# Kernel optimization log

Measured on AMD Instinct MI355X. Metric: run time of the kernel, lower is better.

The kernel has to match this reference:

```python
import jax, jax.numpy as jnp
import numpy as np

B, T, E, H, D = 4, 2048, 1024, 16, 64  # batch, seq(block_size), n_embed, num_heads, hidden_dim


def setup_inputs() -> dict:
    key = jax.random.key(0)
    ks = jax.random.split(key, 10)
    s_in = 1.0 / np.sqrt(E)
    return {
        "x": jax.random.normal(ks[0], (B, T, E), dtype=jnp.float32),
        "Wq": jax.random.normal(ks[1], (H, E, D), dtype=jnp.float32) * s_in,
        "bq": jnp.zeros((H, D), dtype=jnp.float32),
        "Wk": jax.random.normal(ks[2], (H, E, D), dtype=jnp.float32) * s_in,
        "bk": jnp.zeros((H, D), dtype=jnp.float32),
        "Wv": jax.random.normal(ks[3], (H, E, D), dtype=jnp.float32) * s_in,
        "bv": jnp.zeros((H, D), dtype=jnp.float32),
        "Wp": jax.random.normal(ks[4], (E, E), dtype=jnp.float32) * s_in,
        "bp": jnp.zeros((E,), dtype=jnp.float32),
    }


def reference(x, Wq, bq, Wk, bk, Wv, bv, Wp, bp):
    # Batched equivalent of the per-head Python loop: each head h computes
    # causal scaled-dot-product attention with its own Q/K/V projections.
    q = jnp.einsum("bte,hed->bhtd", x, Wq) + bq[None, :, None, :]
    k = jnp.einsum("bte,hed->bhtd", x, Wk) + bk[None, :, None, :]
    v = jnp.einsum("bte,hed->bhtd", x, Wv) + bv[None, :, None, :]
    scale = 1.0 / jnp.sqrt(jnp.asarray(D, dtype=x.dtype))
    scores = jnp.einsum("bhtd,bhsd->bhts", q, k) * scale  # [B,H,T,T]
    causal = jnp.tril(jnp.ones((T, T), dtype=bool))
    scores = jnp.where(causal[None, None, :, :], scores, jnp.asarray(-jnp.inf, dtype=x.dtype))
    att = jax.nn.softmax(scores, axis=-1)
    head_out = jnp.einsum("bhts,bhsd->bhtd", att, v)  # [B,H,T,D]
    # concat heads along last dim: [B,T,H*D] == [B,T,E]
    cat = head_out.transpose(0, 2, 1, 3).reshape(B, T, H * D)
    out = cat @ Wp + bp  # final projection (dropout is identity in eval)
    return out
```

## Files before the change

kernel.cpp:

```cpp
#include <hip/hip_runtime.h>


typedef __attribute__((ext_vector_type(8))) __bf16 bf16x8;
typedef __attribute__((ext_vector_type(4))) float f32x4;
typedef __attribute__((ext_vector_type(16))) float f32x16;
typedef __attribute__((ext_vector_type(4))) unsigned int u32x4;
typedef __attribute__((ext_vector_type(2))) unsigned int u32x2;
typedef unsigned short u16;
typedef unsigned int u32;

#define DEV __device__ __forceinline__

#define QK_SCALE 0.18033688011112042f

DEV u16 f2bf(float f) {
  u32 u = __builtin_bit_cast(u32, f);
  u += 0x7fffu + ((u >> 16) & 1u);
  return (u16)(u >> 16);
}
DEV u32 pack2(float a, float b) { return (u32)f2bf(a) | ((u32)f2bf(b) << 16); }

DEV float exp2_hw(float x) { float r; asm("v_exp_f32 %0, %1" : "=v"(r) : "v"(x)); return r; }
DEV u32 cvtpk_bf16(float lo, float hi) {
  u32 r; asm("v_cvt_pk_bf16_f32 %0, %1, %2" : "=v"(r) : "v"(lo), "v"(hi)); return r;
}
DEV void pl32swap(u32& a, u32& b) { asm("v_permlane32_swap_b32 %0, %1" : "+v"(a), "+v"(b)); }
DEV float max3f(float a, float b, float c) {
  float r; asm("v_max3_f32 %0, %1, %2, %3" : "=v"(r) : "v"(a), "v"(b), "v"(c)); return r;
}

DEV f32x16 zero16() { f32x16 z;
#pragma unroll
  for (int i = 0; i < 16; i++) z[i] = 0.f;
  return z; }

DEV void gll16(const u16* g, u16* l) {
  __builtin_amdgcn_global_load_lds((const __attribute__((address_space(1))) void*)g,
                                   (__attribute__((address_space(3))) void*)l, 16, 0, 0);
}

#define SCHEDB() __builtin_amdgcn_sched_barrier(0)
#define FENCE4()  do { asm volatile("s_waitcnt vmcnt(4) lgkmcnt(0)" ::: "memory"); SCHEDB(); \
                       __builtin_amdgcn_s_barrier(); SCHEDB(); } while (0)
#define FENCE0()  do { asm volatile("s_waitcnt vmcnt(0) lgkmcnt(0)" ::: "memory"); SCHEDB(); \
                       __builtin_amdgcn_s_barrier(); SCHEDB(); } while (0)

__global__ __launch_bounds__(256) void prep_all_kernel(
    const float* __restrict__ x, const float* __restrict__ bq, const float* __restrict__ bk,
    const float* __restrict__ bv, const float* __restrict__ Wq, const float* __restrict__ Wk,
    const float* __restrict__ Wv, const float* __restrict__ Wp,
    u16* __restrict__ xbf, float* __restrict__ bqkv, u16* __restrict__ wqkvT, u16* __restrict__ wpT) {
  __shared__ float t[64][65];
  int bidAll = blockIdx.x, tid = threadIdx.x;
  if (bidAll < 4096) {
    int gid = bidAll * 256 + tid;
    if (gid < 3072) {
      float v = (gid < 1024) ? bq[gid] * QK_SCALE : (gid < 2048 ? bk[gid - 1024] : bv[gid - 2048]);
      bqkv[gid] = v;
    }
    const float4* xv = (const float4*)x;
    float4 f0 = xv[(size_t)gid * 2];
    float4 f1 = xv[(size_t)gid * 2 + 1];
    u32x4 st;
    st.x = pack2(f0.x, f0.y); st.y = pack2(f0.z, f0.w);
    st.z = pack2(f1.x, f1.y); st.w = pack2(f1.z, f1.w);
    *(u32x4*)&xbf[(size_t)gid * 8] = st;
    return;
  }
  int bid = bidAll - 4096;
  int r0 = tid >> 6, c = tid & 63;
  if (bid < 768) {
    int p = bid >> 8, rem = bid & 255, h = rem >> 4, et = rem & 15;
    float sc = (p == 0) ? QK_SCALE : 1.0f;
    const float* src = (p == 0 ? Wq : (p == 1 ? Wk : Wv)) + ((size_t)h * 1024 + et * 64) * 64;
#pragma unroll
    for (int i = 0; i < 16; i++) { int e = r0 + i * 4; t[e][c] = src[(size_t)e * 64 + c]; }
    __syncthreads();
    u16* dst = wqkvT + ((size_t)p * 1024 + h * 64) * 1024 + et * 64;
#pragma unroll
    for (int i = 0; i < 16; i++) { int d = r0 + i * 4; dst[(size_t)d * 1024 + c] = f2bf(t[c][d] * sc); }
  } else {
    int b2 = bid - 768, rt = b2 >> 4, ct = b2 & 15;
#pragma unroll
    for (int i = 0; i < 16; i++) { int e = r0 + i * 4; t[e][c] = Wp[(size_t)(rt * 64 + e) * 1024 + ct * 64 + c]; }
    __syncthreads();
#pragma unroll
    for (int i = 0; i < 16; i++) { int f = r0 + i * 4; wpT[(size_t)(ct * 64 + f) * 1024 + rt * 64 + c] = f2bf(t[c][f]); }
  }
}

DEV void stage_tile32(const u16* __restrict__ X, int row0, int k0, u16* lds, int tid) {
#pragma unroll
  for (int j = 0; j < 2; j++) {
    int ci = j * 256 + tid;
    int L = ci >> 3, half = (ci >> 2) & 1, s = ci & 3;
    int row = L * 2 + half;
    int srcslot = s ^ (L & 3);
    gll16(X + (size_t)(row0 + row) * 1024 + k0 + srcslot * 8, lds + ci * 8);
  }
}

DEV int frag_off32(int row, int lg) {
  return (row >> 1) * 64 + (row & 1) * 32 + ((lg ^ ((row >> 1) & 3)) * 8);
}

__global__ __launch_bounds__(256, 3) void gemm128_kernel(
    const u16* __restrict__ A, const u16* __restrict__ Bt, const float* __restrict__ bias,
    int tilesN, int mode, u16* __restrict__ Qb, u16* __restrict__ Kb, u16* __restrict__ VTb,
    float* __restrict__ outF) {
  __shared__ u16 As[3][128 * 32];
  __shared__ u16 Bs[3][128 * 32];
  int nwg = gridDim.x;
  int bid = blockIdx.x;
  int swz = (bid % 8) * (nwg / 8) + bid / 8;
  int bm = swz / tilesN, bn = swz % tilesN;
  int tid = threadIdx.x;
  int lane = tid & 63, wave = tid >> 6;
  int wm = wave >> 1, wn = wave & 1;
  int lr = lane & 15, lg = lane >> 4;

  f32x4 acc[4][4];
#pragma unroll
  for (int i = 0; i < 4; i++)
#pragma unroll
    for (int j = 0; j < 4; j++) acc[i][j] = f32x4{0.f, 0.f, 0.f, 0.f};

  int aoff[4], boff[4];
#pragma unroll
  for (int i = 0; i < 4; i++) {
    aoff[i] = frag_off32(wm * 64 + i * 16 + lr, lg);
    boff[i] = frag_off32(wn * 64 + i * 16 + lr, lg);
  }

  stage_tile32(A, bm * 128, 0, As[0], tid);
  stage_tile32(Bt, bn * 128, 0, Bs[0], tid);
  stage_tile32(A, bm * 128, 32, As[1], tid);
  stage_tile32(Bt, bn * 128, 32, Bs[1], tid);
  asm volatile("s_waitcnt vmcnt(4)" ::: "memory");
  SCHEDB();
  __builtin_amdgcn_s_barrier();
  SCHEDB();

  int rs = 0;
  for (int t = 0; t < 32; ++t) {
    int ws = rs + 2; if (ws >= 3) ws -= 3;
    bool st = (t + 2) < 32;
    if (st) {
      stage_tile32(A, bm * 128, (t + 2) * 32, As[ws], tid);
      stage_tile32(Bt, bn * 128, (t + 2) * 32, Bs[ws], tid);
    }
    bf16x8 af[4], bfr[4];
#pragma unroll
    for (int i = 0; i < 4; i++) {
      af[i] = *(const bf16x8*)&As[rs][aoff[i]];
      bfr[i] = *(const bf16x8*)&Bs[rs][boff[i]];
    }
    __builtin_amdgcn_s_setprio(1);
#pragma unroll
    for (int i = 0; i < 4; i++)
#pragma unroll
      for (int j = 0; j < 4; j++)
        acc[i][j] = __builtin_amdgcn_mfma_f32_16x16x32_bf16(af[i], bfr[j], acc[i][j], 0, 0, 0);
    __builtin_amdgcn_s_setprio(0);
    if (st) FENCE4(); else FENCE0();
    rs = rs + 1; if (rs >= 3) rs -= 3;
  }

  int crow = bm * 128 + wm * 64;
  int ccol = bn * 128 + wn * 64;
  if (mode == 0) {
#pragma unroll
    for (int j = 0; j < 4; j++) {
      int col = ccol + j * 16 + lr;
      float bb = bias[col];
      int p = col >> 10, h = (col >> 6) & 15, d = col & 63;
#pragma unroll
      for (int i = 0; i < 4; i++) {
        int row0 = crow + i * 16 + lg * 4;
        int b_ = row0 >> 11, t0 = row0 & 2047;
        if (p == 2) {
          u32x2 pv;
          pv.x = pack2(acc[i][j][0] + bb, acc[i][j][1] + bb);
          pv.y = pack2(acc[i][j][2] + bb, acc[i][j][3] + bb);
          *(u32x2*)&VTb[((size_t)(b_ * 16 + h) * 64 + d) * 2048 + t0] = pv;
        } else {
          u16* dst = (p == 0 ? Qb : Kb);
#pragma unroll
          for (int r = 0; r < 4; r++)
            dst[((size_t)(b_ * 16 + h) * 2048 + (t0 + r)) * 64 + d] = f2bf(acc[i][j][r] + bb);
        }
      }
    }
  } else {
#pragma unroll
    for (int j = 0; j < 4; j++) {
      int col = ccol + j * 16 + lr;
      float bb = bias[col];
#pragma unroll
      for (int i = 0; i < 4; i++) {
        int row0 = crow + i * 16 + lg * 4;
#pragma unroll
        for (int r = 0; r < 4; r++)
          outF[(size_t)(row0 + r) * 1024 + col] = acc[i][j][r] + bb;
      }
    }
  }
}

DEV void stage_kv256(const u16* __restrict__ Kh, const u16* __restrict__ Vh, int kv0,
                     u16* Ksb, u16* Vsb, int tid) {
#pragma unroll
  for (int j = 0; j < 2; j++) {
    int ci = j * 256 + tid;
    int row = ci >> 3, slot = ci & 7;
    int ss = slot ^ (row & 7);
    gll16(Kh + (size_t)(kv0 + row) * 64 + ss * 8, Ksb + ci * 8);
    gll16(Vh + (size_t)row * 2048 + kv0 + ss * 8, Vsb + ci * 8);
  }
}

__global__ __launch_bounds__(256, 2) void attn_kernel(
    const u16* __restrict__ Qb, const u16* __restrict__ Kb, const u16* __restrict__ VTb,
    u16* __restrict__ cat) {
  __shared__ u16 Ks[3][64 * 64];
  __shared__ u16 Vs[3][64 * 64];
  int bid = blockIdx.x;
  int t = 15 - (bid >> 6);
  int bh = bid & 63;
  int b = bh >> 4, h = bh & 15;
  int tid = threadIdx.x, wave = tid >> 6, lane = tid & 63;
  int l31 = lane & 31, hi = lane >> 5;
  int q0w = t * 128 + wave * 32;
  int qrow = q0w + l31;

  const u16* Qh = Qb + (size_t)bh * 2048 * 64;
  const u16* Kh = Kb + (size_t)bh * 2048 * 64;
  const u16* Vh = VTb + (size_t)bh * 64 * 2048;

  bf16x8 qf[4];
#pragma unroll
  for (int ks = 0; ks < 4; ks++)
    qf[ks] = *(const bf16x8*)&Qh[(size_t)qrow * 64 + ks * 16 + hi * 8];

  u32 loff[4];
#pragma unroll
  for (int ks = 0; ks < 4; ks++)
    loff[ks] = (u32)(l31 * 128 + (((ks * 2 + hi) ^ (l31 & 7)) * 16));

  f32x16 o0 = zero16(), o1 = zero16();
  float m_run = -1e30f, l_run = 0.f;
  int iters = 2 * t + 2;

  stage_kv256(Kh, Vh, 0, Ks[0], Vs[0], tid);
  stage_kv256(Kh, Vh, 64, Ks[1], Vs[1], tid);
  asm volatile("s_waitcnt vmcnt(4)" ::: "memory");
  SCHEDB();
  __builtin_amdgcn_s_barrier();
  SCHEDB();

  int rs = 0;
  for (int kvt = 0; kvt < iters; ++kvt) {
    int kv0 = kvt * 64;
    int ws = rs + 2; if (ws >= 3) ws -= 3;
    bool st = (kvt + 2) < iters;
    if (st) stage_kv256(Kh, Vh, kv0 + 128, Ks[ws], Vs[ws], tid);

    if (kv0 <= q0w + 31) {
      f32x16 s0 = zero16(), s1 = zero16();
      const char* kb = (const char*)&Ks[rs][0];
      __builtin_amdgcn_s_setprio(1);
#pragma unroll
      for (int ks = 0; ks < 4; ks++) {
        bf16x8 k0 = *(const bf16x8*)(kb + loff[ks]);
        bf16x8 k1 = *(const bf16x8*)(kb + loff[ks] + 4096);
        s0 = __builtin_amdgcn_mfma_f32_32x32x16_bf16(k0, qf[ks], s0, 0, 0, 0);
        s1 = __builtin_amdgcn_mfma_f32_32x32x16_bf16(k1, qf[ks], s1, 0, 0, 0);
      }
      __builtin_amdgcn_s_setprio(0);

      if (kv0 + 63 > q0w) {
        int relh = qrow - kv0 - 4 * hi;
#pragma unroll
        for (int r = 0; r < 16; r++) {
          int off = (r & 3) + 8 * (r >> 2);
          s0[r] = (off > relh) ? -1e30f : s0[r];
          s1[r] = (off + 32 > relh) ? -1e30f : s1[r];
        }
      }

      float ta = max3f(s0[0], s0[1], s0[2]);
      float tb = max3f(s0[4], s0[5], s0[6]);
      float tc = max3f(s0[8], s0[9], s0[10]);
      float td = max3f(s0[12], s0[13], s0[14]);
      ta = max3f(ta, s0[3], s1[0]);
      tb = max3f(tb, s0[7], s1[4]);
      tc = max3f(tc, s0[11], s1[8]);
      td = max3f(td, s0[15], s1[12]);
      ta = max3f(ta, s1[1], s1[2]);
      tb = max3f(tb, s1[5], s1[6]);
      tc = max3f(tc, s1[9], s1[10]);
      td = max3f(td, s1[13], s1[14]);
      ta = max3f(ta, s1[3], tb);
      tc = max3f(tc, s1[7], td);
      float tmax = max3f(ta, tc, s1[11]);
      tmax = fmaxf(tmax, s1[15]);
      tmax = fmaxf(tmax, __shfl_xor(tmax, 32));
      float corr = 1.f;
      if (!__all(tmax <= m_run + 8.f)) {
        float m_new = fmaxf(m_run, tmax);
        corr = exp2_hw(m_run - m_new);
        o0 = o0 * corr;
        o1 = o1 * corr;
        m_run = m_new;
      }
      float t0 = 0.f, t1 = 0.f, t2 = 0.f, t3 = 0.f;
#pragma unroll
      for (int j = 0; j < 4; j++) {
        float p00 = exp2_hw(s0[j * 4 + 0] - m_run); s0[j * 4 + 0] = p00; t0 += p00;
        float p01 = exp2_hw(s0[j * 4 + 1] - m_run); s0[j * 4 + 1] = p01; t1 += p01;
        float p02 = exp2_hw(s0[j * 4 + 2] - m_run); s0[j * 4 + 2] = p02; t2 += p02;
        float p03 = exp2_hw(s0[j * 4 + 3] - m_run); s0[j * 4 + 3] = p03; t3 += p03;
        float p10 = exp2_hw(s1[j * 4 + 0] - m_run); s1[j * 4 + 0] = p10; t0 += p10;
        float p11 = exp2_hw(s1[j * 4 + 1] - m_run); s1[j * 4 + 1] = p11; t1 += p11;
        float p12 = exp2_hw(s1[j * 4 + 2] - m_run); s1[j * 4 + 2] = p12; t2 += p12;
        float p13 = exp2_hw(s1[j * 4 + 3] - m_run); s1[j * 4 + 3] = p13; t3 += p13;
      }
      float ts = (t0 + t1) + (t2 + t3);
      ts += __shfl_xor(ts, 32);
      l_run = l_run * corr + ts;

      const char* vb = (const char*)&Vs[rs][0];
      __builtin_amdgcn_s_setprio(1);
#pragma unroll
      for (int ks = 0; ks < 4; ks++) {
        const f32x16& sb = (ks < 2) ? s0 : s1;
        int g2 = (ks & 1) * 8;
        u32 a  = cvtpk_bf16(sb[g2 + 0], sb[g2 + 1]);
        u32 c  = cvtpk_bf16(sb[g2 + 2], sb[g2 + 3]);
        u32 bb = cvtpk_bf16(sb[g2 + 4], sb[g2 + 5]);
        u32 d  = cvtpk_bf16(sb[g2 + 6], sb[g2 + 7]);
        pl32swap(a, bb);
        pl32swap(c, d);
        u32x4 wv; wv.x = a; wv.y = c; wv.z = bb; wv.w = d;
        bf16x8 pf = __builtin_bit_cast(bf16x8, wv);
        bf16x8 v0 = *(const bf16x8*)(vb + loff[ks]);
        bf16x8 v1 = *(const bf16x8*)(vb + loff[ks] + 4096);
        o0 = __builtin_amdgcn_mfma_f32_32x32x16_bf16(v0, pf, o0, 0, 0, 0);
        o1 = __builtin_amdgcn_mfma_f32_32x32x16_bf16(v1, pf, o1, 0, 0, 0);
      }
      __builtin_amdgcn_s_setprio(0);
    }

    if (st) FENCE4(); else FENCE0();
    rs = rs + 1; if (rs >= 3) rs -= 3;
  }

  float li = 1.0f / l_run;
#pragma unroll
  for (int m = 0; m < 8; m++) {
    int dbase = 2 * (m & 1) + 8 * (m >> 1) + 4 * hi;
    u32 w0 = cvtpk_bf16(o0[2 * m] * li, o0[2 * m + 1] * li);
    u32 w1 = cvtpk_bf16(o1[2 * m] * li, o1[2 * m + 1] * li);
    *(u32*)&cat[(size_t)(b * 2048 + qrow) * 1024 + h * 64 + dbase] = w0;
    *(u32*)&cat[(size_t)(b * 2048 + qrow) * 1024 + h * 64 + 32 + dbase] = w1;
  }
}

extern "C" void kernel_launch(void* const* d_in, const int* in_sizes, int n_in,
                              void* d_out, int out_size, void* d_ws, size_t ws_size,
                              hipStream_t stream) {
  const float* x  = (const float*)d_in[0];
  const float* Wq = (const float*)d_in[1];
  const float* bq = (const float*)d_in[2];
  const float* Wk = (const float*)d_in[3];
  const float* bk = (const float*)d_in[4];
  const float* Wv = (const float*)d_in[5];
  const float* bv = (const float*)d_in[6];
  const float* Wp = (const float*)d_in[7];
  const float* bp = (const float*)d_in[8];

  char* w = (char*)d_ws;
  u16* xbf    = (u16*)w;                 w += (size_t)8192 * 1024 * 2;
  u16* wqkvT  = (u16*)w;                 w += (size_t)3072 * 1024 * 2;
  u16* wpT    = (u16*)w;                 w += (size_t)1024 * 1024 * 2;
  float* bqkv = (float*)w;               w += (size_t)3072 * 4;
  u16* Qb     = (u16*)w;                 w += (size_t)64 * 2048 * 64 * 2;
  u16* Kb     = (u16*)w;                 w += (size_t)64 * 2048 * 64 * 2;
  u16* VTb    = (u16*)w;                 w += (size_t)64 * 64 * 2048 * 2;
  u16* cat    = (u16*)w;                 w += (size_t)8192 * 1024 * 2;

  prep_all_kernel<<<5120, 256, 0, stream>>>(x, bq, bk, bv, Wq, Wk, Wv, Wp, xbf, bqkv, wqkvT, wpT);
  gemm128_kernel<<<1536, 256, 0, stream>>>(xbf, wqkvT, bqkv, 24, 0, Qb, Kb, VTb, nullptr);
  attn_kernel<<<1024, 256, 0, stream>>>(Qb, Kb, VTb, cat);
  gemm128_kernel<<<512, 256, 0, stream>>>(cat, wpT, bp, 8, 1, nullptr, nullptr, nullptr, (float*)d_out);
}
```

Baseline: 158.7 us.

## Restructure GEMM to two waves with 128x64 per-wave tiles and double buffering

The 128x128 GEMM tile now runs with 128 threads (2 waves) instead of 256. Each wave covers 128 rows by 64 columns, giving 32 MFMA accumulators per wave. The triple-buffered LDS pipeline with explicit vmcnt fences is replaced by simple double buffering with __syncthreads, which halves LDS use. The goal is more register-level reuse of A fragments per wave, at the cost of fewer waves to hide latency and a shallower prefetch pipeline.

```diff
diff --git a/kernel.cpp b/kernel.cpp
--- a/kernel.cpp
+++ b/kernel.cpp
@@ -91,8 +91,8 @@
 
 DEV void stage_tile32(const u16* __restrict__ X, int row0, int k0, u16* lds, int tid) {
 #pragma unroll
-  for (int j = 0; j < 2; j++) {
-    int ci = j * 256 + tid;
+  for (int j = 0; j < 4; j++) {
+    int ci = j * 128 + tid;
     int L = ci >> 3, half = (ci >> 2) & 1, s = ci & 3;
     int row = L * 2 + half;
     int srcslot = s ^ (L & 3);
@@ -104,79 +104,69 @@
   return (row >> 1) * 64 + (row & 1) * 32 + ((lg ^ ((row >> 1) & 3)) * 8);
 }
 
-__global__ __launch_bounds__(256, 3) void gemm128_kernel(
+__global__ __launch_bounds__(128, 2) void gemm128_kernel(
     const u16* __restrict__ A, const u16* __restrict__ Bt, const float* __restrict__ bias,
     int tilesN, int mode, u16* __restrict__ Qb, u16* __restrict__ Kb, u16* __restrict__ VTb,
     float* __restrict__ outF) {
-  __shared__ u16 As[3][128 * 32];
-  __shared__ u16 Bs[3][128 * 32];
+  __shared__ u16 As[2][128 * 32];
+  __shared__ u16 Bs[2][128 * 32];
   int nwg = gridDim.x;
   int bid = blockIdx.x;
   int swz = (bid % 8) * (nwg / 8) + bid / 8;
   int bm = swz / tilesN, bn = swz % tilesN;
   int tid = threadIdx.x;
-  int lane = tid & 63, wave = tid >> 6;
-  int wm = wave >> 1, wn = wave & 1;
+  int lane = tid & 63;
+  int wn = tid >> 6;
   int lr = lane & 15, lg = lane >> 4;
 
-  f32x4 acc[4][4];
-#pragma unroll
-  for (int i = 0; i < 4; i++)
+  f32x4 acc[8][4];
+#pragma unroll
+  for (int i = 0; i < 8; i++)
 #pragma unroll
     for (int j = 0; j < 4; j++) acc[i][j] = f32x4{0.f, 0.f, 0.f, 0.f};
 
-  int aoff[4], boff[4];
-#pragma unroll
-  for (int i = 0; i < 4; i++) {
-    aoff[i] = frag_off32(wm * 64 + i * 16 + lr, lg);
-    boff[i] = frag_off32(wn * 64 + i * 16 + lr, lg);
-  }
+  int aoff[8], boff[4];
+#pragma unroll
+  for (int i = 0; i < 8; i++) aoff[i] = frag_off32(i * 16 + lr, lg);
+#pragma unroll
+  for (int j = 0; j < 4; j++) boff[j] = frag_off32(wn * 64 + j * 16 + lr, lg);
 
   stage_tile32(A, bm * 128, 0, As[0], tid);
   stage_tile32(Bt, bn * 128, 0, Bs[0], tid);
-  stage_tile32(A, bm * 128, 32, As[1], tid);
-  stage_tile32(Bt, bn * 128, 32, Bs[1], tid);
-  asm volatile("s_waitcnt vmcnt(4)" ::: "memory");
-  SCHEDB();
-  __builtin_amdgcn_s_barrier();
-  SCHEDB();
-
-  int rs = 0;
+  __syncthreads();
+  int cur = 0;
+
   for (int t = 0; t < 32; ++t) {
-    int ws = rs + 2; if (ws >= 3) ws -= 3;
-    bool st = (t + 2) < 32;
-    if (st) {
-      stage_tile32(A, bm * 128, (t + 2) * 32, As[ws], tid);
-      stage_tile32(Bt, bn * 128, (t + 2) * 32, Bs[ws], tid);
-    }
-    bf16x8 af[4], bfr[4];
-#pragma unroll
-    for (int i = 0; i < 4; i++) {
-      af[i] = *(const bf16x8*)&As[rs][aoff[i]];
-      bfr[i] = *(const bf16x8*)&Bs[rs][boff[i]];
-    }
+    if (t + 1 < 32) {
+      stage_tile32(A, bm * 128, (t + 1) * 32, As[cur ^ 1], tid);
+      stage_tile32(Bt, bn * 128, (t + 1) * 32, Bs[cur ^ 1], tid);
+    }
+    bf16x8 af[8], bfr[4];
+#pragma unroll
+    for (int i = 0; i < 8; i++) af[i] = *(const bf16x8*)&As[cur][aoff[i]];
+#pragma unroll
+    for (int j = 0; j < 4; j++) bfr[j] = *(const bf16x8*)&Bs[cur][boff[j]];
     __builtin_amdgcn_s_setprio(1);
 #pragma unroll
-    for (int i = 0; i < 4; i++)
+    for (int i = 0; i < 8; i++)
 #pragma unroll
       for (int j = 0; j < 4; j++)
         acc[i][j] = __builtin_amdgcn_mfma_f32_16x16x32_bf16(af[i], bfr[j], acc[i][j], 0, 0, 0);
     __builtin_amdgcn_s_setprio(0);
-    if (st) FENCE4(); else FENCE0();
-    rs = rs + 1; if (rs >= 3) rs -= 3;
-  }
-
-  int crow = bm * 128 + wm * 64;
-  int ccol = bn * 128 + wn * 64;
+    __syncthreads();
+    cur ^= 1;
+  }
+
+  int ccolb = bn * 128 + wn * 64;
   if (mode == 0) {
 #pragma unroll
     for (int j = 0; j < 4; j++) {
-      int col = ccol + j * 16 + lr;
+      int col = ccolb + j * 16 + lr;
       float bb = bias[col];
       int p = col >> 10, h = (col >> 6) & 15, d = col & 63;
 #pragma unroll
-      for (int i = 0; i < 4; i++) {
-        int row0 = crow + i * 16 + lg * 4;
+      for (int i = 0; i < 8; i++) {
+        int row0 = bm * 128 + i * 16 + lg * 4;
         int b_ = row0 >> 11, t0 = row0 & 2047;
         if (p == 2) {
           u32x2 pv;
@@ -194,11 +184,11 @@
   } else {
 #pragma unroll
     for (int j = 0; j < 4; j++) {
-      int col = ccol + j * 16 + lr;
+      int col = ccolb + j * 16 + lr;
       float bb = bias[col];
 #pragma unroll
-      for (int i = 0; i < 4; i++) {
-        int row0 = crow + i * 16 + lg * 4;
+      for (int i = 0; i < 8; i++) {
+        int row0 = bm * 128 + i * 16 + lg * 4;
 #pragma unroll
         for (int r = 0; r < 4; r++)
           outF[(size_t)(row0 + r) * 1024 + col] = acc[i][j][r] + bb;
@@ -390,7 +380,7 @@
   u16* cat    = (u16*)w;                 w += (size_t)8192 * 1024 * 2;
 
   prep_all_kernel<<<5120, 256, 0, stream>>>(x, bq, bk, bv, Wq, Wk, Wv, Wp, xbf, bqkv, wqkvT, wpT);
-  gemm128_kernel<<<1536, 256, 0, stream>>>(xbf, wqkvT, bqkv, 24, 0, Qb, Kb, VTb, nullptr);
+  gemm128_kernel<<<1536, 128, 0, stream>>>(xbf, wqkvT, bqkv, 24, 0, Qb, Kb, VTb, nullptr);
   attn_kernel<<<1024, 256, 0, stream>>>(Qb, Kb, VTb, cat);
-  gemm128_kernel<<<512, 256, 0, stream>>>(cat, wpT, bp, 8, 1, nullptr, nullptr, nullptr, (float*)d_out);
-}
+  gemm128_kernel<<<512, 128, 0, stream>>>(cat, wpT, bp, 8, 1, nullptr, nullptr, nullptr, (float*)d_out);
+}
```

Result: slower. 169.4 us (+6.7%).
